# Kernel optimization log

Hardware: AMD Instinct MI355X
Metric: run time of the kernel (lower is better)

Reference implementation:

```python
import jax, jax.numpy as jnp
import numpy as np

N = 384          # nodes per graph
HID = 128        # hid_dim
H = 8            # shared_num_heads
C = HID // H     # shared_head_dim = 16
L = 4            # num_layers
VOCAB = 20
NORB = 4
NCAT = NORB * NORB + NORB   # 20 edge categories
OUT = 10
B = 4
E = N * N        # fully-connected closure incl. self loops
EPS = 1e-5


def layer_norm(x, g, b):
    m = jnp.mean(x, axis=-1, keepdims=True)
    v = jnp.mean((x - m) ** 2, axis=-1, keepdims=True)
    return (x - m) / jnp.sqrt(v + EPS) * g + b


def setup_inputs() -> dict:
    key = jax.random.key(0)
    ks = iter(jax.random.split(key, 32))

    def nrm(shape, s=0.05):
        return jax.random.normal(next(ks), shape, jnp.float32) * s

    # edge structure: fully connected, edge (i,j) in row-major order
    pos = np.arange(N) % NORB                    # node -> orbit
    src = np.repeat(np.arange(N), N)
    tgt = np.tile(np.arange(N), N)
    cat = np.where(src == tgt, NORB * NORB + pos[src], pos[src] * NORB + pos[tgt])

    x = jax.random.randint(next(ks), (B, N, 1), 0, VOCAB, jnp.int32)

    return dict(
        x=x,
        edge_src=jnp.asarray(src, jnp.int32),
        edge_tgt=jnp.asarray(tgt, jnp.int32),
        edge_cat=jnp.asarray(cat, jnp.int32),
        token_emb=nrm((VOCAB, HID), 1.0),
        edge_emb=nrm((NCAT, HID), 1.0),
        ln_in1_g=jnp.ones((HID,), jnp.float32), ln_in1_b=jnp.zeros((HID,), jnp.float32),
        W_in=nrm((HID, HID)), b_in=jnp.zeros((HID,), jnp.float32),
        ln_in2_g=jnp.ones((HID,), jnp.float32), ln_in2_b=jnp.zeros((HID,), jnp.float32),
        Wl=nrm((L, HID, H * C)), bl=jnp.zeros((L, H * C), jnp.float32),
        Wr=nrm((L, HID, H * C)), br=jnp.zeros((L, H * C), jnp.float32),
        We=nrm((L, HID, H * C)),                           # lin_edge has no bias in PyG GATv2Conv
        att=nrm((L, H, C)),
        bias_gat=jnp.zeros((L, H * C), jnp.float32),
        W_proj=nrm((L, HID, HID)), b_proj=jnp.zeros((L, HID), jnp.float32),
        ln_g=jnp.ones((L, HID), jnp.float32), ln_b=jnp.zeros((L, HID), jnp.float32),
        W_out=nrm((HID, OUT)), b_out=jnp.zeros((OUT,), jnp.float32),
    )


def reference(x, edge_src, edge_tgt, edge_cat,
              token_emb, edge_emb,
              ln_in1_g, ln_in1_b, W_in, b_in, ln_in2_g, ln_in2_b,
              Wl, bl, Wr, br, We, att, bias_gat,
              W_proj, b_proj, ln_g, ln_b, W_out, b_out):
    edge_feat = edge_emb[edge_cat]                       # [E, HID] gather by category
    h = token_emb[x[..., 0]]                             # [B, N, HID]
    # input MLP: LN -> ReLU -> Linear -> LN
    h = layer_norm(h, ln_in1_g, ln_in1_b)
    h = jax.nn.relu(h)
    h = h @ W_in + b_in
    h = layer_norm(h, ln_in2_g, ln_in2_b)

    for l in range(L):
        edge_e = (edge_feat @ We[l]).reshape(E, H, C)    # shared across batch

        def conv(hb):  # hb: [N, HID]  GATv2Conv, concat heads
            xl = (hb @ Wl[l] + bl[l]).reshape(N, H, C)   # source transform
            xr = (hb @ Wr[l] + br[l]).reshape(N, H, C)   # target transform
            e = jax.nn.leaky_relu(xl[edge_src] + xr[edge_tgt] + edge_e, 0.2)  # [E,H,C]
            logits = jnp.einsum('ehc,hc->eh', e, att[l])                      # [E,H]
            # segment softmax over edges sharing a target node
            m = jax.ops.segment_max(logits, edge_tgt, num_segments=N)
            ex = jnp.exp(logits - m[edge_tgt])
            den = jax.ops.segment_sum(ex, edge_tgt, num_segments=N)
            alpha = ex / den[edge_tgt]                                        # [E,H]
            out = jax.ops.segment_sum(xl[edge_src] * alpha[:, :, None], edge_tgt,
                                      num_segments=N)                         # [N,H,C]
            return out.reshape(N, H * C) + bias_gat[l]

        h_prev = h
        h = jax.vmap(conv)(h)                            # [B, N, HID]
        h = h @ W_proj[l] + b_proj[l]
        h = layer_norm(h, ln_g[l], ln_b[l])
        h = jax.nn.relu(h) + h_prev                      # residual

    h = h.sum(axis=1)                                    # sum over nodes -> [B, HID]
    return h @ W_out + b_out                             # [B, OUT]
```

## Files before the change

kernel.cpp:

```cpp
#include <hip/hip_runtime.h>


#define NN 384
#define NB 4
#define TJ 3

__device__ __forceinline__ void reduce32(float& a, float& b) {
#pragma unroll
  for (int m = 1; m <= 16; m <<= 1) {
    a += __shfl_xor(a, m, 64);
    b += __shfl_xor(b, m, 64);
  }
}

__global__ __launch_bounds__(256) void k_init(
    const int* __restrict__ x,
    const float* __restrict__ token_emb, const float* __restrict__ edge_emb,
    const float* __restrict__ ln1g, const float* __restrict__ ln1b,
    const float* __restrict__ W_in, const float* __restrict__ b_in,
    const float* __restrict__ ln2g, const float* __restrict__ ln2b,
    const float* __restrict__ Wl, const float* __restrict__ bl,
    const float* __restrict__ Wr, const float* __restrict__ br,
    const float* __restrict__ We, const float* __restrict__ att_w,
    float* __restrict__ ce, float* __restrict__ h,
    float* __restrict__ xl, float* __restrict__ xr, float* __restrict__ datt0)
{
  const int blk = blockIdx.x, t = threadIdx.x;
  if (blk < 40) {
    const int idx = blk * 256 + t;
    const int hc = idx & 127, rest = idx >> 7;
    const int cat = rest % 20, l = rest / 20;
    const float* er = edge_emb + cat * 128;
    const float* w  = We + (l * 128) * 128 + hc;
    float acc = 0.f;
#pragma unroll 8
    for (int k = 0; k < 128; ++k) acc = fmaf(er[k], w[k * 128], acc);
    ce[idx] = acc;
    return;
  }
  __shared__ float trow[8][128];
  __shared__ float hbuf[8][128];
  const int r0 = (blk - 40) * 8;
  const int r = t >> 5, cw = (t & 31) * 4;
  const int row = r0 + r;
  const int tok = x[row];
  float4 v = *(const float4*)(token_emb + tok * 128 + cw);
  float s1 = v.x + v.y + v.z + v.w;
  float s2 = v.x * v.x + v.y * v.y + v.z * v.z + v.w * v.w;
  reduce32(s1, s2);
  float mean = s1 * 0.0078125f;
  float inv  = rsqrtf(s2 * 0.0078125f - mean * mean + 1e-5f);
  {
    float4 g  = *(const float4*)(ln1g + cw);
    float4 bb = *(const float4*)(ln1b + cw);
    trow[r][cw + 0] = fmaxf((v.x - mean) * inv * g.x + bb.x, 0.f);
    trow[r][cw + 1] = fmaxf((v.y - mean) * inv * g.y + bb.y, 0.f);
    trow[r][cw + 2] = fmaxf((v.z - mean) * inv * g.z + bb.z, 0.f);
    trow[r][cw + 3] = fmaxf((v.w - mean) * inv * g.w + bb.w, 0.f);
  }
  __syncthreads();
  const int o = t & 127, rh = (t >> 7) * 4;
  float a0, a1, a2, a3;
  { float bo = b_in[o]; a0 = a1 = a2 = a3 = bo; }
  for (int k = 0; k < 128; ++k) {
    float w = W_in[k * 128 + o];
    a0 = fmaf(trow[rh + 0][k], w, a0);
    a1 = fmaf(trow[rh + 1][k], w, a1);
    a2 = fmaf(trow[rh + 2][k], w, a2);
    a3 = fmaf(trow[rh + 3][k], w, a3);
  }
  hbuf[rh + 0][o] = a0; hbuf[rh + 1][o] = a1;
  hbuf[rh + 2][o] = a2; hbuf[rh + 3][o] = a3;
  __syncthreads();
  v = *(const float4*)(&hbuf[r][cw]);
  s1 = v.x + v.y + v.z + v.w;
  s2 = v.x * v.x + v.y * v.y + v.z * v.z + v.w * v.w;
  reduce32(s1, s2);
  mean = s1 * 0.0078125f;
  inv  = rsqrtf(s2 * 0.0078125f - mean * mean + 1e-5f);
  {
    float4 g  = *(const float4*)(ln2g + cw);
    float4 bb = *(const float4*)(ln2b + cw);
    float4 hv;
    hv.x = (v.x - mean) * inv * g.x + bb.x;
    hv.y = (v.y - mean) * inv * g.y + bb.y;
    hv.z = (v.z - mean) * inv * g.z + bb.z;
    hv.w = (v.w - mean) * inv * g.w + bb.w;
    *(float4*)(&trow[r][cw]) = hv;
    *(float4*)(h + row * 128 + cw) = hv;
  }
  __syncthreads();
  float l0, l1, l2, l3, q0, q1, q2, q3;
  { float blo = bl[o], bro = br[o]; l0 = l1 = l2 = l3 = blo; q0 = q1 = q2 = q3 = bro; }
  for (int k = 0; k < 128; ++k) {
    float wl = Wl[k * 128 + o], wr = Wr[k * 128 + o];
    float h0 = trow[rh + 0][k], h1 = trow[rh + 1][k];
    float h2 = trow[rh + 2][k], h3 = trow[rh + 3][k];
    l0 = fmaf(h0, wl, l0); q0 = fmaf(h0, wr, q0);
    l1 = fmaf(h1, wl, l1); q1 = fmaf(h1, wr, q1);
    l2 = fmaf(h2, wl, l2); q2 = fmaf(h2, wr, q2);
    l3 = fmaf(h3, wl, l3); q3 = fmaf(h3, wr, q3);
  }
  const int rb = r0 + rh;
  xl[(rb + 0) * 128 + o] = l0; xr[(rb + 0) * 128 + o] = q0;
  xl[(rb + 1) * 128 + o] = l1; xr[(rb + 1) * 128 + o] = q1;
  xl[(rb + 2) * 128 + o] = l2; xr[(rb + 2) * 128 + o] = q2;
  xl[(rb + 3) * 128 + o] = l3; xr[(rb + 3) * 128 + o] = q3;
  {
    float av = att_w[o];
    float s0 = av * l0, sA = av * l1, sB = av * l2, sC = av * l3;
#pragma unroll
    for (int mm = 1; mm <= 8; mm <<= 1) {
      s0 += __shfl_xor(s0, mm, 64);
      sA += __shfl_xor(sA, mm, 64);
      sB += __shfl_xor(sB, mm, 64);
      sC += __shfl_xor(sC, mm, 64);
    }
    if ((t & 15) == 0) {
      const int hh2 = o >> 4;
      const int bb2 = r0 / NN, ii = r0 - bb2 * NN + rh;
      const int base = (bb2 * 8 + hh2) * NN + ii;
      datt0[base + 0] = s0; datt0[base + 1] = sA;
      datt0[base + 2] = sB; datt0[base + 3] = sC;
    }
  }
}

__global__ __launch_bounds__(256) void k_layer(
    const float* __restrict__ xl_in, const float* __restrict__ xr_in,
    const float* __restrict__ datt_in,
    float* __restrict__ xl_out, float* __restrict__ xr_out,
    float* __restrict__ datt_out,
    float* __restrict__ h, const float* __restrict__ ce,
    const float* __restrict__ att_w, const float* __restrict__ bias_gat,
    const float* __restrict__ W_proj, const float* __restrict__ b_proj,
    const float* __restrict__ ln_g, const float* __restrict__ ln_b,
    const float* __restrict__ Wl, const float* __restrict__ bl,
    const float* __restrict__ Wr, const float* __restrict__ br,
    int l, int next_l)
{
  __shared__ float xrce[TJ][5][136];
  __shared__ float djr02[TJ][5][8];
  __shared__ float mbuf[8][32][17];
  __shared__ float arow[TJ][132];
  __shared__ float pbuf[2 * TJ][132];
  __shared__ float nrow[TJ][132];

  const int blk = blockIdx.x, t = threadIdx.x;
  const int jt = blk & 127, b = blk >> 7;
  const int j0 = jt * TJ;

  for (int idx = t; idx < TJ * 5 * 128; idx += 256) {
    const int hc = idx & 127, rest = idx >> 7;
    const int sel = rest % 5, jj = rest / 5;
    const int j = j0 + jj, pj = j & 3;
    const int cat = (sel == 4) ? (16 + pj) : (sel * 4 + pj);
    xrce[jj][sel][hc] = xr_in[(b * NN + j) * 128 + hc] + ce[(l * 20 + cat) * 128 + hc];
  }
  __syncthreads();
  if (t < TJ * 5 * 8) {
    const int jj = t / 40, r2 = t % 40, sel = r2 >> 3, h2 = r2 & 7;
    float d = 0.f;
#pragma unroll
    for (int c = 0; c < 16; ++c)
      d += xrce[jj][sel][h2 * 16 + c] * att_w[l * 128 + h2 * 16 + c];
    djr02[jj][sel][h2] = 0.2f * d;
  }
  __syncthreads();

  const int hh = t >> 5, isub = t & 31;
  float attv[16];
  {
    const float* ap = att_w + l * 128 + hh * 16;
#pragma unroll
    for (int c = 0; c < 16; ++c) attv[c] = ap[c];
  }
  float sden[TJ];
  float acc[TJ][16];
#pragma unroll
  for (int jj = 0; jj < TJ; ++jj) {
    sden[jj] = 0.f;
#pragma unroll
    for (int c = 0; c < 16; ++c) acc[jj][c] = 0.f;
  }
  const float* xlb = xl_in + (b * NN) * 128 + hh * 16;
  const float* dp  = datt_in + (b * 8 + hh) * NN;

  for (int it = 0; it < NN / 32; ++it) {
    const int i = isub + 32 * it;
    float xv[16];
    {
      const float4* xp = (const float4*)(xlb + i * 128);
#pragma unroll
      for (int q = 0; q < 4; ++q) {
        float4 a = xp[q];
        xv[q * 4 + 0] = a.x; xv[q * 4 + 1] = a.y;
        xv[q * 4 + 2] = a.z; xv[q * 4 + 3] = a.w;
      }
    }
    const float di02 = 0.2f * dp[i];
    const int pi = i & 3;
#pragma unroll
    for (int jj = 0; jj < TJ; ++jj) {
      const int sel = (i == j0 + jj) ? 4 : pi;
      const float4* bp = (const float4*)(&xrce[jj][sel][hh * 16]);
      float p = 0.f;
#pragma unroll
      for (int q = 0; q < 4; ++q) {
        float4 cv = bp[q];
        p = fmaf(fmaxf(xv[q * 4 + 0] + cv.x, 0.f), attv[q * 4 + 0], p);
        p = fmaf(fmaxf(xv[q * 4 + 1] + cv.y, 0.f), attv[q * 4 + 1], p);
        p = fmaf(fmaxf(xv[q * 4 + 2] + cv.z, 0.f), attv[q * 4 + 2], p);
        p = fmaf(fmaxf(xv[q * 4 + 3] + cv.w, 0.f), attv[q * 4 + 3], p);
      }
      const float e = __expf(fmaf(0.8f, p, di02 + djr02[jj][sel][hh]));
      sden[jj] += e;
#pragma unroll
      for (int c = 0; c < 16; ++c) acc[jj][c] = fmaf(e, xv[c], acc[jj][c]);
    }
  }

  for (int jj = 0; jj < TJ; ++jj) {
    __syncthreads();
    mbuf[hh][isub][0] = sden[jj];
#pragma unroll
    for (int c = 0; c < 16; ++c) mbuf[hh][isub][1 + c] = acc[jj][c];
    __syncthreads();
    if (t < 128) {
      const int h2 = t >> 4, c2 = t & 15;
      float den = 0.f, num = 0.f;
#pragma unroll 8
      for (int u = 0; u < 32; ++u) {
        den += mbuf[h2][u][0];
        num += mbuf[h2][u][1 + c2];
      }
      arow[jj][t] = num / den + bias_gat[l * 128 + t];
    }
  }
  __syncthreads();

  {
    const int o = t & 127, half = t >> 7;
    const float* Wp = W_proj + l * 16384;
    float p0 = 0.f, p1 = 0.f, p2 = 0.f;
    const int k0 = half * 64;
    for (int kk = 0; kk < 64; ++kk) {
      const int k = k0 + kk;
      const float w = Wp[k * 128 + o];
      p0 = fmaf(arow[0][k], w, p0);
      p1 = fmaf(arow[1][k], w, p1);
      p2 = fmaf(arow[2][k], w, p2);
    }
    pbuf[half * 3 + 0][o] = p0;
    pbuf[half * 3 + 1][o] = p1;
    pbuf[half * 3 + 2][o] = p2;
  }
  __syncthreads();
  if (t < 128) {
    const float bo = b_proj[l * 128 + t];
    nrow[0][t] = pbuf[0][t] + pbuf[3][t] + bo;
    nrow[1][t] = pbuf[1][t] + pbuf[4][t] + bo;
    nrow[2][t] = pbuf[2][t] + pbuf[5][t] + bo;
  }
  __syncthreads();

  {
    const int w = t >> 6;
    if (w < TJ) {
      const int c2 = (t & 63) * 2;
      float v0 = nrow[w][c2], v1 = nrow[w][c2 + 1];
      float s1 = v0 + v1, s2 = v0 * v0 + v1 * v1;
#pragma unroll
      for (int m = 1; m <= 32; m <<= 1) {
        s1 += __shfl_xor(s1, m, 64);
        s2 += __shfl_xor(s2, m, 64);
      }
      const float mean = s1 * 0.0078125f;
      const float inv  = rsqrtf(s2 * 0.0078125f - mean * mean + 1e-5f);
      const int row = (b * NN + j0 + w) * 128;
      const float g0 = ln_g[l * 128 + c2], g1 = ln_g[l * 128 + c2 + 1];
      const float b0 = ln_b[l * 128 + c2], b1 = ln_b[l * 128 + c2 + 1];
      const float hp0 = h[row + c2], hp1 = h[row + c2 + 1];
      const float hn0 = fmaxf((v0 - mean) * inv * g0 + b0, 0.f) + hp0;
      const float hn1 = fmaxf((v1 - mean) * inv * g1 + b1, 0.f) + hp1;
      h[row + c2] = hn0; h[row + c2 + 1] = hn1;
      nrow[w][c2] = hn0; nrow[w][c2 + 1] = hn1;
    }
  }
  __syncthreads();

  if (next_l >= 0) {
    const int o = t & 127, m = t >> 7;
    const float* W = (m ? Wr : Wl) + next_l * 16384;
    const float bias = (m ? br : bl)[next_l * 128 + o];
    float a0 = bias, a1 = bias, a2 = bias;
    for (int k = 0; k < 128; ++k) {
      const float wv = W[k * 128 + o];
      a0 = fmaf(nrow[0][k], wv, a0);
      a1 = fmaf(nrow[1][k], wv, a1);
      a2 = fmaf(nrow[2][k], wv, a2);
    }
    float* dst = m ? xr_out : xl_out;
    const int rb = (b * NN + j0) * 128 + o;
    dst[rb] = a0; dst[rb + 128] = a1; dst[rb + 256] = a2;
    if (m == 0) {
      const float av = att_w[next_l * 128 + o];
      float s0 = av * a0, s1 = av * a1, s2 = av * a2;
#pragma unroll
      for (int mm = 1; mm <= 8; mm <<= 1) {
        s0 += __shfl_xor(s0, mm, 64);
        s1 += __shfl_xor(s1, mm, 64);
        s2 += __shfl_xor(s2, mm, 64);
      }
      if ((t & 15) == 0) {
        const int base = (b * 8 + (o >> 4)) * NN + j0;
        datt_out[base + 0] = s0;
        datt_out[base + 1] = s1;
        datt_out[base + 2] = s2;
      }
    }
  }
}

__global__ __launch_bounds__(256) void k_final(
    const float* __restrict__ h, const float* __restrict__ W_out,
    const float* __restrict__ b_out, float* __restrict__ out)
{
  __shared__ float sbuf[2][128];
  const int bq = blockIdx.x, t = threadIdx.x;
  const int o = t & 127, half = t >> 7;
  float acc = 0.f;
  const float* hp = h + (bq * NN + half * 192) * 128 + o;
  for (int n = 0; n < 192; ++n) acc += hp[n * 128];
  sbuf[half][o] = acc;
  __syncthreads();
  if (t < 10) {
    float a = b_out[t];
#pragma unroll 8
    for (int k = 0; k < 128; ++k)
      a = fmaf(sbuf[0][k] + sbuf[1][k], W_out[k * 10 + t], a);
    out[bq * 10 + t] = a;
  }
}

extern "C" void kernel_launch(void* const* d_in, const int* in_sizes, int n_in,
                              void* d_out, int out_size, void* d_ws, size_t ws_size,
                              hipStream_t stream) {
  const int*   x         = (const int*)d_in[0];
  const float* token_emb = (const float*)d_in[4];
  const float* edge_emb  = (const float*)d_in[5];
  const float* ln1g      = (const float*)d_in[6];
  const float* ln1b      = (const float*)d_in[7];
  const float* W_in      = (const float*)d_in[8];
  const float* b_in      = (const float*)d_in[9];
  const float* ln2g      = (const float*)d_in[10];
  const float* ln2b      = (const float*)d_in[11];
  const float* Wl        = (const float*)d_in[12];
  const float* bl        = (const float*)d_in[13];
  const float* Wr        = (const float*)d_in[14];
  const float* br        = (const float*)d_in[15];
  const float* We        = (const float*)d_in[16];
  const float* att_w     = (const float*)d_in[17];
  const float* bias_gat  = (const float*)d_in[18];
  const float* W_proj    = (const float*)d_in[19];
  const float* b_proj    = (const float*)d_in[20];
  const float* ln_g      = (const float*)d_in[21];
  const float* ln_b      = (const float*)d_in[22];
  const float* W_out     = (const float*)d_in[23];
  const float* b_out     = (const float*)d_in[24];

  float* ws  = (float*)d_ws;
  float* ce  = ws;
  float* h   = ce  + 10240;
  float* xlA = h   + 196608;
  float* xrA = xlA + 196608;
  float* xlB = xrA + 196608;
  float* xrB = xlB + 196608;
  float* dA  = xrB + 196608;
  float* dB  = dA  + 12288;

  k_init<<<dim3(40 + 192), 256, 0, stream>>>(
      x, token_emb, edge_emb, ln1g, ln1b, W_in, b_in, ln2g, ln2b,
      Wl, bl, Wr, br, We, att_w, ce, h, xlA, xrA, dA);
  for (int l = 0; l < 4; ++l) {
    const bool even = (l & 1) == 0;
    float* xin  = even ? xlA : xlB;  float* rin  = even ? xrA : xrB;
    float* din  = even ? dA  : dB;
    float* xout = even ? xlB : xlA;  float* rout = even ? xrB : xrA;
    float* dout = even ? dB  : dA;
    k_layer<<<dim3(NB * (NN / TJ)), 256, 0, stream>>>(
        xin, rin, din, xout, rout, dout, h, ce, att_w, bias_gat,
        W_proj, b_proj, ln_g, ln_b, Wl, bl, Wr, br, l, (l < 3) ? l + 1 : -1);
  }
  k_final<<<dim3(NB), 256, 0, stream>>>(h, W_out, b_out, (float*)d_out);
}
```

Baseline: 230.5 us.

## Shrink target tile to two nodes, prefetch source rows, restructure init kernel

Lowers the number of target nodes per block from three to two, so k_layer launches 768 blocks instead of 512, which gives the GPU more parallel blocks. The main attention loop now prefetches the next source row of xl and its attention scalar into registers, hiding global load latency behind the current iteration's math. k_init is rewritten to process two rows per block, using split-K matmuls and wave-wide layernorm reductions in the same style as k_layer, and k_final uses two accumulators. The trade-off is more redundant per-block setup (xr+ce staging, weight reads) per useful output row, plus extra registers for the prefetch buffers.

```diff
diff --git a/kernel.cpp b/kernel.cpp
--- a/kernel.cpp
+++ b/kernel.cpp
@@ -3,15 +3,7 @@
 
 #define NN 384
 #define NB 4
-#define TJ 3
-
-__device__ __forceinline__ void reduce32(float& a, float& b) {
-#pragma unroll
-  for (int m = 1; m <= 16; m <<= 1) {
-    a += __shfl_xor(a, m, 64);
-    b += __shfl_xor(b, m, 64);
-  }
-}
+#define TJ 2
 
 __global__ __launch_bounds__(256) void k_init(
     const int* __restrict__ x,
@@ -38,90 +30,99 @@
     ce[idx] = acc;
     return;
   }
-  __shared__ float trow[8][128];
-  __shared__ float hbuf[8][128];
-  const int r0 = (blk - 40) * 8;
-  const int r = t >> 5, cw = (t & 31) * 4;
-  const int row = r0 + r;
-  const int tok = x[row];
-  float4 v = *(const float4*)(token_emb + tok * 128 + cw);
-  float s1 = v.x + v.y + v.z + v.w;
-  float s2 = v.x * v.x + v.y * v.y + v.z * v.z + v.w * v.w;
-  reduce32(s1, s2);
-  float mean = s1 * 0.0078125f;
-  float inv  = rsqrtf(s2 * 0.0078125f - mean * mean + 1e-5f);
-  {
-    float4 g  = *(const float4*)(ln1g + cw);
-    float4 bb = *(const float4*)(ln1b + cw);
-    trow[r][cw + 0] = fmaxf((v.x - mean) * inv * g.x + bb.x, 0.f);
-    trow[r][cw + 1] = fmaxf((v.y - mean) * inv * g.y + bb.y, 0.f);
-    trow[r][cw + 2] = fmaxf((v.z - mean) * inv * g.z + bb.z, 0.f);
-    trow[r][cw + 3] = fmaxf((v.w - mean) * inv * g.w + bb.w, 0.f);
-  }
-  __syncthreads();
-  const int o = t & 127, rh = (t >> 7) * 4;
-  float a0, a1, a2, a3;
-  { float bo = b_in[o]; a0 = a1 = a2 = a3 = bo; }
-  for (int k = 0; k < 128; ++k) {
-    float w = W_in[k * 128 + o];
-    a0 = fmaf(trow[rh + 0][k], w, a0);
-    a1 = fmaf(trow[rh + 1][k], w, a1);
-    a2 = fmaf(trow[rh + 2][k], w, a2);
-    a3 = fmaf(trow[rh + 3][k], w, a3);
-  }
-  hbuf[rh + 0][o] = a0; hbuf[rh + 1][o] = a1;
-  hbuf[rh + 2][o] = a2; hbuf[rh + 3][o] = a3;
-  __syncthreads();
-  v = *(const float4*)(&hbuf[r][cw]);
-  s1 = v.x + v.y + v.z + v.w;
-  s2 = v.x * v.x + v.y * v.y + v.z * v.z + v.w * v.w;
-  reduce32(s1, s2);
-  mean = s1 * 0.0078125f;
-  inv  = rsqrtf(s2 * 0.0078125f - mean * mean + 1e-5f);
-  {
-    float4 g  = *(const float4*)(ln2g + cw);
-    float4 bb = *(const float4*)(ln2b + cw);
-    float4 hv;
-    hv.x = (v.x - mean) * inv * g.x + bb.x;
-    hv.y = (v.y - mean) * inv * g.y + bb.y;
-    hv.z = (v.z - mean) * inv * g.z + bb.z;
-    hv.w = (v.w - mean) * inv * g.w + bb.w;
-    *(float4*)(&trow[r][cw]) = hv;
-    *(float4*)(h + row * 128 + cw) = hv;
-  }
-  __syncthreads();
-  float l0, l1, l2, l3, q0, q1, q2, q3;
-  { float blo = bl[o], bro = br[o]; l0 = l1 = l2 = l3 = blo; q0 = q1 = q2 = q3 = bro; }
-  for (int k = 0; k < 128; ++k) {
-    float wl = Wl[k * 128 + o], wr = Wr[k * 128 + o];
-    float h0 = trow[rh + 0][k], h1 = trow[rh + 1][k];
-    float h2 = trow[rh + 2][k], h3 = trow[rh + 3][k];
-    l0 = fmaf(h0, wl, l0); q0 = fmaf(h0, wr, q0);
-    l1 = fmaf(h1, wl, l1); q1 = fmaf(h1, wr, q1);
-    l2 = fmaf(h2, wl, l2); q2 = fmaf(h2, wr, q2);
-    l3 = fmaf(h3, wl, l3); q3 = fmaf(h3, wr, q3);
-  }
-  const int rb = r0 + rh;
-  xl[(rb + 0) * 128 + o] = l0; xr[(rb + 0) * 128 + o] = q0;
-  xl[(rb + 1) * 128 + o] = l1; xr[(rb + 1) * 128 + o] = q1;
-  xl[(rb + 2) * 128 + o] = l2; xr[(rb + 2) * 128 + o] = q2;
-  xl[(rb + 3) * 128 + o] = l3; xr[(rb + 3) * 128 + o] = q3;
-  {
-    float av = att_w[o];
-    float s0 = av * l0, sA = av * l1, sB = av * l2, sC = av * l3;
-#pragma unroll
-    for (int mm = 1; mm <= 8; mm <<= 1) {
-      s0 += __shfl_xor(s0, mm, 64);
-      sA += __shfl_xor(sA, mm, 64);
-      sB += __shfl_xor(sB, mm, 64);
-      sC += __shfl_xor(sC, mm, 64);
-    }
-    if ((t & 15) == 0) {
-      const int hh2 = o >> 4;
-      const int bb2 = r0 / NN, ii = r0 - bb2 * NN + rh;
-      const int base = (bb2 * 8 + hh2) * NN + ii;
-      datt0[base + 0] = s0; datt0[base + 1] = sA;
-      datt0[base + 2] = sB; datt0[base + 3] = sC;
+  __shared__ float arow[TJ][132];
+  __shared__ float pbuf[2 * TJ][132];
+  __shared__ float nrow[TJ][132];
+  const int gr0 = (blk - 40) * TJ;
+  const int b = gr0 / NN, j0 = gr0 - b * NN;
+
+  {
+    const int w = t >> 6;
+    if (w < TJ) {
+      const int c2 = (t & 63) * 2;
+      const int tok = x[gr0 + w];
+      const float* te = token_emb + tok * 128;
+      float v0 = te[c2], v1 = te[c2 + 1];
+      float s1 = v0 + v1, s2 = v0 * v0 + v1 * v1;
+#pragma unroll
+      for (int m = 1; m <= 32; m <<= 1) {
+        s1 += __shfl_xor(s1, m, 64);
+        s2 += __shfl_xor(s2, m, 64);
+      }
+      const float mean = s1 * 0.0078125f;
+      const float inv  = rsqrtf(s2 * 0.0078125f - mean * mean + 1e-5f);
+      arow[w][c2]     = fmaxf((v0 - mean) * inv * ln1g[c2]     + ln1b[c2],     0.f);
+      arow[w][c2 + 1] = fmaxf((v1 - mean) * inv * ln1g[c2 + 1] + ln1b[c2 + 1], 0.f);
+    }
+  }
+  __syncthreads();
+  {
+    const int o = t & 127, half = t >> 7, k0 = half * 64;
+    float p0 = 0.f, p1 = 0.f;
+#pragma unroll 4
+    for (int kk = 0; kk < 64; ++kk) {
+      const int k = k0 + kk;
+      const float w = W_in[k * 128 + o];
+      p0 = fmaf(arow[0][k], w, p0);
+      p1 = fmaf(arow[1][k], w, p1);
+    }
+    pbuf[half * TJ + 0][o] = p0;
+    pbuf[half * TJ + 1][o] = p1;
+  }
+  __syncthreads();
+  if (t < 128) {
+    const float bo = b_in[t];
+    nrow[0][t] = pbuf[0][t] + pbuf[TJ][t] + bo;
+    nrow[1][t] = pbuf[1][t] + pbuf[TJ + 1][t] + bo;
+  }
+  __syncthreads();
+  {
+    const int w = t >> 6;
+    if (w < TJ) {
+      const int c2 = (t & 63) * 2;
+      float v0 = nrow[w][c2], v1 = nrow[w][c2 + 1];
+      float s1 = v0 + v1, s2 = v0 * v0 + v1 * v1;
+#pragma unroll
+      for (int m = 1; m <= 32; m <<= 1) {
+        s1 += __shfl_xor(s1, m, 64);
+        s2 += __shfl_xor(s2, m, 64);
+      }
+      const float mean = s1 * 0.0078125f;
+      const float inv  = rsqrtf(s2 * 0.0078125f - mean * mean + 1e-5f);
+      const float hn0 = (v0 - mean) * inv * ln2g[c2]     + ln2b[c2];
+      const float hn1 = (v1 - mean) * inv * ln2g[c2 + 1] + ln2b[c2 + 1];
+      const int row = (gr0 + w) * 128;
+      h[row + c2] = hn0; h[row + c2 + 1] = hn1;
+      nrow[w][c2] = hn0; nrow[w][c2 + 1] = hn1;
+    }
+  }
+  __syncthreads();
+  {
+    const int o = t & 127, m = t >> 7;
+    const float* W = (m ? Wr : Wl);
+    const float bias = (m ? br : bl)[o];
+    float a0 = bias, a1 = bias;
+#pragma unroll 4
+    for (int k = 0; k < 128; ++k) {
+      const float wv = W[k * 128 + o];
+      a0 = fmaf(nrow[0][k], wv, a0);
+      a1 = fmaf(nrow[1][k], wv, a1);
+    }
+    float* dst = m ? xr : xl;
+    const int rb = gr0 * 128 + o;
+    dst[rb] = a0; dst[rb + 128] = a1;
+    if (m == 0) {
+      const float av = att_w[o];
+      float s0 = av * a0, s1 = av * a1;
+#pragma unroll
+      for (int mm = 1; mm <= 8; mm <<= 1) {
+        s0 += __shfl_xor(s0, mm, 64);
+        s1 += __shfl_xor(s1, mm, 64);
+      }
+      if ((t & 15) == 0) {
+        const int base = (b * 8 + (o >> 4)) * NN + j0;
+        datt0[base] = s0; datt0[base + 1] = s1;
+      }
     }
   }
 }
@@ -140,15 +141,16 @@
     int l, int next_l)
 {
   __shared__ float xrce[TJ][5][136];
-  __shared__ float djr02[TJ][5][8];
-  __shared__ float mbuf[8][32][17];
+  __shared__ float djr02s[TJ][5][8];
+  __shared__ float mbuf[8][545];
   __shared__ float arow[TJ][132];
   __shared__ float pbuf[2 * TJ][132];
   __shared__ float nrow[TJ][132];
 
   const int blk = blockIdx.x, t = threadIdx.x;
-  const int jt = blk & 127, b = blk >> 7;
+  const int jt = blk % (NN / TJ), b = blk / (NN / TJ);
   const int j0 = jt * TJ;
+  const int gr0 = b * NN + j0;
 
   for (int idx = t; idx < TJ * 5 * 128; idx += 256) {
     const int hc = idx & 127, rest = idx >> 7;
@@ -164,7 +166,7 @@
 #pragma unroll
     for (int c = 0; c < 16; ++c)
       d += xrce[jj][sel][h2 * 16 + c] * att_w[l * 128 + h2 * 16 + c];
-    djr02[jj][sel][h2] = 0.2f * d;
+    djr02s[jj][sel][h2] = 0.2f * d;
   }
   __syncthreads();
 
@@ -186,19 +188,30 @@
   const float* xlb = xl_in + (b * NN) * 128 + hh * 16;
   const float* dp  = datt_in + (b * 8 + hh) * NN;
 
+  float xv[16], di02;
+  {
+    const float4* xp = (const float4*)(xlb + isub * 128);
+#pragma unroll
+    for (int q = 0; q < 4; ++q) {
+      float4 a = xp[q];
+      xv[q * 4 + 0] = a.x; xv[q * 4 + 1] = a.y;
+      xv[q * 4 + 2] = a.z; xv[q * 4 + 3] = a.w;
+    }
+    di02 = 0.2f * dp[isub];
+  }
   for (int it = 0; it < NN / 32; ++it) {
     const int i = isub + 32 * it;
-    float xv[16];
-    {
-      const float4* xp = (const float4*)(xlb + i * 128);
+    float nxv[16], ndi = 0.f;
+    if (it < NN / 32 - 1) {
+      const float4* xp = (const float4*)(xlb + (i + 32) * 128);
 #pragma unroll
       for (int q = 0; q < 4; ++q) {
         float4 a = xp[q];
-        xv[q * 4 + 0] = a.x; xv[q * 4 + 1] = a.y;
-        xv[q * 4 + 2] = a.z; xv[q * 4 + 3] = a.w;
-      }
-    }
-    const float di02 = 0.2f * dp[i];
+        nxv[q * 4 + 0] = a.x; nxv[q * 4 + 1] = a.y;
+        nxv[q * 4 + 2] = a.z; nxv[q * 4 + 3] = a.w;
+      }
+      ndi = 0.2f * dp[i + 32];
+    }
     const int pi = i & 3;
 #pragma unroll
     for (int jj = 0; jj < TJ; ++jj) {
@@ -213,26 +226,29 @@
         p = fmaf(fmaxf(xv[q * 4 + 2] + cv.z, 0.f), attv[q * 4 + 2], p);
         p = fmaf(fmaxf(xv[q * 4 + 3] + cv.w, 0.f), attv[q * 4 + 3], p);
       }
-      const float e = __expf(fmaf(0.8f, p, di02 + djr02[jj][sel][hh]));
+      const float e = __expf(fmaf(0.8f, p, di02 + djr02s[jj][sel][hh]));
       sden[jj] += e;
 #pragma unroll
       for (int c = 0; c < 16; ++c) acc[jj][c] = fmaf(e, xv[c], acc[jj][c]);
     }
+#pragma unroll
+    for (int c = 0; c < 16; ++c) xv[c] = nxv[c];
+    di02 = ndi;
   }
 
   for (int jj = 0; jj < TJ; ++jj) {
     __syncthreads();
-    mbuf[hh][isub][0] = sden[jj];
-#pragma unroll
-    for (int c = 0; c < 16; ++c) mbuf[hh][isub][1 + c] = acc[jj][c];
+    mbuf[hh][isub * 17] = sden[jj];
+#pragma unroll
+    for (int c = 0; c < 16; ++c) mbuf[hh][isub * 17 + 1 + c] = acc[jj][c];
     __syncthreads();
     if (t < 128) {
       const int h2 = t >> 4, c2 = t & 15;
       float den = 0.f, num = 0.f;
 #pragma unroll 8
       for (int u = 0; u < 32; ++u) {
-        den += mbuf[h2][u][0];
-        num += mbuf[h2][u][1 + c2];
+        den += mbuf[h2][u * 17];
+        num += mbuf[h2][u * 17 + 1 + c2];
       }
       arow[jj][t] = num / den + bias_gat[l * 128 + t];
     }
@@ -240,27 +256,24 @@
   __syncthreads();
 
   {
-    const int o = t & 127, half = t >> 7;
+    const int o = t & 127, half = t >> 7, k0 = half * 64;
     const float* Wp = W_proj + l * 16384;
-    float p0 = 0.f, p1 = 0.f, p2 = 0.f;
-    const int k0 = half * 64;
+    float p0 = 0.f, p1 = 0.f;
+#pragma unroll 4
     for (int kk = 0; kk < 64; ++kk) {
       const int k = k0 + kk;
       const float w = Wp[k * 128 + o];
       p0 = fmaf(arow[0][k], w, p0);
       p1 = fmaf(arow[1][k], w, p1);
-      p2 = fmaf(arow[2][k], w, p2);
-    }
-    pbuf[half * 3 + 0][o] = p0;
-    pbuf[half * 3 + 1][o] = p1;
-    pbuf[half * 3 + 2][o] = p2;
+    }
+    pbuf[half * TJ + 0][o] = p0;
+    pbuf[half * TJ + 1][o] = p1;
   }
   __syncthreads();
   if (t < 128) {
     const float bo = b_proj[l * 128 + t];
-    nrow[0][t] = pbuf[0][t] + pbuf[3][t] + bo;
-    nrow[1][t] = pbuf[1][t] + pbuf[4][t] + bo;
-    nrow[2][t] = pbuf[2][t] + pbuf[5][t] + bo;
+    nrow[0][t] = pbuf[0][t] + pbuf[TJ][t] + bo;
+    nrow[1][t] = pbuf[1][t] + pbuf[TJ + 1][t] + bo;
   }
   __syncthreads();
 
@@ -277,7 +290,7 @@
       }
       const float mean = s1 * 0.0078125f;
       const float inv  = rsqrtf(s2 * 0.0078125f - mean * mean + 1e-5f);
-      const int row = (b * NN + j0 + w) * 128;
+      const int row = (gr0 + w) * 128;
       const float g0 = ln_g[l * 128 + c2], g1 = ln_g[l * 128 + c2 + 1];
       const float b0 = ln_b[l * 128 + c2], b1 = ln_b[l * 128 + c2 + 1];
       const float hp0 = h[row + c2], hp1 = h[row + c2 + 1];
@@ -293,30 +306,27 @@
     const int o = t & 127, m = t >> 7;
     const float* W = (m ? Wr : Wl) + next_l * 16384;
     const float bias = (m ? br : bl)[next_l * 128 + o];
-    float a0 = bias, a1 = bias, a2 = bias;
+    float a0 = bias, a1 = bias;
+#pragma unroll 4
     for (int k = 0; k < 128; ++k) {
       const float wv = W[k * 128 + o];
       a0 = fmaf(nrow[0][k], wv, a0);
       a1 = fmaf(nrow[1][k], wv, a1);
-      a2 = fmaf(nrow[2][k], wv, a2);
     }
     float* dst = m ? xr_out : xl_out;
-    const int rb = (b * NN + j0) * 128 + o;
-    dst[rb] = a0; dst[rb + 128] = a1; dst[rb + 256] = a2;
+    const int rb = gr0 * 128 + o;
+    dst[rb] = a0; dst[rb + 128] = a1;
     if (m == 0) {
       const float av = att_w[next_l * 128 + o];
-      float s0 = av * a0, s1 = av * a1, s2 = av * a2;
+      float s0 = av * a0, s1 = av * a1;
 #pragma unroll
       for (int mm = 1; mm <= 8; mm <<= 1) {
         s0 += __shfl_xor(s0, mm, 64);
         s1 += __shfl_xor(s1, mm, 64);
-        s2 += __shfl_xor(s2, mm, 64);
       }
       if ((t & 15) == 0) {
         const int base = (b * 8 + (o >> 4)) * NN + j0;
-        datt_out[base + 0] = s0;
-        datt_out[base + 1] = s1;
-        datt_out[base + 2] = s2;
+        datt_out[base] = s0; datt_out[base + 1] = s1;
       }
     }
   }
@@ -329,10 +339,13 @@
   __shared__ float sbuf[2][128];
   const int bq = blockIdx.x, t = threadIdx.x;
   const int o = t & 127, half = t >> 7;
-  float acc = 0.f;
+  float acc0 = 0.f, acc1 = 0.f;
   const float* hp = h + (bq * NN + half * 192) * 128 + o;
-  for (int n = 0; n < 192; ++n) acc += hp[n * 128];
-  sbuf[half][o] = acc;
+  for (int n = 0; n < 96; ++n) {
+    acc0 += hp[(2 * n) * 128];
+    acc1 += hp[(2 * n + 1) * 128];
+  }
+  sbuf[half][o] = acc0 + acc1;
   __syncthreads();
   if (t < 10) {
     float a = b_out[t];
@@ -379,7 +392,7 @@
   float* dA  = xrB + 196608;
   float* dB  = dA  + 12288;
 
-  k_init<<<dim3(40 + 192), 256, 0, stream>>>(
+  k_init<<<dim3(40 + NB * NN / TJ), 256, 0, stream>>>(
       x, token_emb, edge_emb, ln1g, ln1b, W_in, b_in, ln2g, ln2b,
       Wl, bl, Wr, br, We, att_w, ce, h, xlA, xrA, dA);
   for (int l = 0; l < 4; ++l) {
```

After: 262.6 us. +13.9%, slower.
